# Optimization experiments

Measured on AMD Instinct MI355X. Metric: run time of the kernel, lower is better.

Reference implementation:

```python
import jax, jax.numpy as jnp
import numpy as np

EPS = 1e-5
NEG_SLOPE = 0.01  # F.leaky_relu default


def setup_inputs() -> dict:
    key = jax.random.key(0)
    k1, k2, k3, k4 = jax.random.split(key, 4)
    N, F, H = 8192, 512, 2
    inputs = jax.random.normal(k1, (N, F), dtype=jnp.float32)
    adj = jnp.zeros((N, N), dtype=jnp.float32)  # accepted but unused by the module
    # torch Linear(F, F*H, bias=False): y = x @ W with W of shape [F, F*H]
    W = jax.random.normal(k2, (F, F * H), dtype=jnp.float32) * (1.0 / np.sqrt(F))
    a_w = jax.random.normal(k3, (1,), dtype=jnp.float32)  # Linear(1,1) weight
    a_b = jax.random.normal(k4, (1,), dtype=jnp.float32)  # Linear(1,1) bias
    return {"inputs": inputs, "adj": adj, "W": W, "a_w": a_w, "a_b": a_b}


def reference(inputs, adj, W, a_w, a_b):
    # Wh, Ws = chunk(inputs @ W, 2)
    WhWs = inputs @ W                       # [N, 2F]
    Wh, Ws = jnp.split(WhWs, 2, axis=-1)    # each [N, F]
    # bias = a(ones) = a_w * 1 + a_b  (constant scalar broadcast)
    bias = (a_w + a_b)[0]
    # dense attention: tanh(Wh + Ws + bias) @ Wh^T  -> [N, N]
    scores = jnp.tanh(Wh + Ws + bias) @ Wh.T
    attn = jax.nn.softmax(scores, axis=-1)  # [N, N]
    out = attn @ Wh + inputs                # [N, F] residual
    # training-mode batch norm over node dim, no affine
    mean = jnp.mean(out, axis=0)
    var = jnp.var(out, axis=0)
    out = (out - mean) * jax.lax.rsqrt(var + EPS)
    return jnp.where(out >= 0, out, NEG_SLOPE * out)
```

## Files before the change

kernel.cpp:

```cpp
#include <hip/hip_runtime.h>

using f32x4 = float    __attribute__((ext_vector_type(4)));
using f16x8 = _Float16 __attribute__((ext_vector_type(8)));
using f16x4 = _Float16 __attribute__((ext_vector_type(4)));

__device__ __forceinline__ void gload_lds16(const void* g, void* l) {
    __builtin_amdgcn_global_load_lds(
        (__attribute__((address_space(1))) void*)(void*)g,
        (__attribute__((address_space(3))) void*)l, 16, 0, 0);
}


__global__ __launch_bounds__(256) void k_cvt_x(
    const float* __restrict__ in, _Float16* __restrict__ out) {
    int i = (blockIdx.x * 256 + threadIdx.x) * 8;
    f32x4 a = *(const f32x4*)(in + i);
    f32x4 b = *(const f32x4*)(in + i + 4);
    f16x8 o;
    #pragma unroll
    for (int j = 0; j < 4; ++j) { o[j] = (_Float16)a[j]; o[j + 4] = (_Float16)b[j]; }
    *(f16x8*)(out + i) = o;
}

__global__ __launch_bounds__(256) void k_cvtT(
    const float* __restrict__ in, _Float16* __restrict__ out, int R, int C) {
    __shared__ _Float16 tile[32][33];
    int c0 = blockIdx.x * 32, r0 = blockIdx.y * 32;
    int tx = threadIdx.x & 31, ty = threadIdx.x >> 5;
    #pragma unroll
    for (int i = ty; i < 32; i += 8)
        tile[i][tx] = (_Float16)in[(size_t)(r0 + i) * C + c0 + tx];
    __syncthreads();
    #pragma unroll
    for (int i = ty; i < 32; i += 8)
        out[(size_t)(c0 + i) * R + r0 + tx] = tile[tx][i];
}

__global__ __launch_bounds__(512, 4) void k_gemm1f(
    const _Float16* __restrict__ A, const _Float16* __restrict__ Bt,
    _Float16* __restrict__ Whh, _Float16* __restrict__ T,
    _Float16* __restrict__ WhT,
    const float* __restrict__ aw, const float* __restrict__ ab) {
    __shared__ _Float16 As[128 * 32];
    __shared__ _Float16 B0s[64 * 32];
    __shared__ _Float16 B1s[64 * 32];
    const float bias = aw[0] + ab[0];
    const int row0 = blockIdx.y * 128, col0 = blockIdx.x * 64;
    const int tid = threadIdx.x, w = tid >> 6, lane = tid & 63;
    const int wm = w >> 2, wn = w & 3;
    const int lrow = lane & 15, quad = lane >> 4;
    const int r16 = lane >> 2;
    const int kc = (((lane & 3) - ((lane >> 3) & 3)) & 3) * 8;
    const int sq = ((quad + ((lrow >> 1) & 3)) & 3) * 8;
    f32x4 acc0[4] = {}, acc1[4] = {};
    for (int k0 = 0; k0 < 512; k0 += 32) {
        gload_lds16(A + (size_t)(row0 + w * 16 + r16) * 512 + k0 + kc,
                    As + w * 512);
        if (w < 4)
            gload_lds16(Bt + (size_t)(col0 + w * 16 + r16) * 512 + k0 + kc,
                        B0s + w * 512);
        else
            gload_lds16(Bt + (size_t)(col0 + 512 + (w - 4) * 16 + r16) * 512 + k0 + kc,
                        B1s + (w - 4) * 512);
        __syncthreads();
        f16x8 af[4], b0, b1;
        #pragma unroll
        for (int i = 0; i < 4; ++i)
            af[i] = *(const f16x8*)(As + (wm * 64 + i * 16 + lrow) * 32 + sq);
        b0 = *(const f16x8*)(B0s + (wn * 16 + lrow) * 32 + sq);
        b1 = *(const f16x8*)(B1s + (wn * 16 + lrow) * 32 + sq);
        #pragma unroll
        for (int mi = 0; mi < 4; ++mi) {
            acc0[mi] = __builtin_amdgcn_mfma_f32_16x16x32_f16(af[mi], b0, acc0[mi], 0, 0, 0);
            acc1[mi] = __builtin_amdgcn_mfma_f32_16x16x32_f16(af[mi], b1, acc1[mi], 0, 0, 0);
        }
        __syncthreads();
    }
    const int col = col0 + wn * 16 + lrow;
    #pragma unroll
    for (int mi = 0; mi < 4; ++mi) {
        int rowb = row0 + wm * 64 + mi * 16 + quad * 4;
        f16x4 pw;
        #pragma unroll
        for (int r = 0; r < 4; ++r) {
            float wh = acc0[mi][r];
            float tt = tanhf(wh + acc1[mi][r] + bias);
            Whh[(size_t)(rowb + r) * 512 + col] = (_Float16)wh;
            T[(size_t)(rowb + r) * 512 + col]   = (_Float16)tt;
            pw[r] = (_Float16)wh;
        }
        *(f16x4*)(WhT + (size_t)col * 8192 + rowb) = pw;
    }
}

__global__ __launch_bounds__(512, 4) void k_gemm2(
    const _Float16* __restrict__ A,
    const _Float16* __restrict__ Bt,
    _Float16* __restrict__ Cp) {
    __shared__ _Float16 As[256 * 64];
    __shared__ _Float16 Bs[128 * 64];
    const int row0 = blockIdx.y * 256, col0 = blockIdx.x * 128;
    const int tid = threadIdx.x, w = tid >> 6, lane = tid & 63;
    const int wm = w >> 1, wn = w & 1;
    const int lrow = lane & 15, quad = lane >> 4;
    const int r8 = lane >> 3;
    const int kc8 = (((lane & 7) - r8) & 7) * 8;
    f32x4 acc[4][4] = {};
    for (int k0 = 0; k0 < 512; k0 += 64) {
        #pragma unroll
        for (int i = 0; i < 6; ++i) {
            int c = w + i * 8;
            if (c < 32) {
                gload_lds16(A + (size_t)(row0 + c * 8 + r8) * 512 + k0 + kc8,
                            As + c * 512);
            } else {
                int c2 = c - 32;
                gload_lds16(Bt + (size_t)(col0 + c2 * 8 + r8) * 512 + k0 + kc8,
                            Bs + c2 * 512);
            }
        }
        __syncthreads();
        #pragma unroll
        for (int ks = 0; ks < 2; ++ks) {
            const int sl = ((quad + ks * 4 + lrow) & 7) * 8;
            f16x8 af[4], bf[4];
            #pragma unroll
            for (int i = 0; i < 4; ++i)
                af[i] = *(const f16x8*)(As + (wm * 64 + i * 16 + lrow) * 64 + sl);
            #pragma unroll
            for (int i = 0; i < 4; ++i)
                bf[i] = *(const f16x8*)(Bs + (wn * 64 + i * 16 + lrow) * 64 + sl);
            #pragma unroll
            for (int mi = 0; mi < 4; ++mi)
                #pragma unroll
                for (int ni = 0; ni < 4; ++ni)
                    acc[mi][ni] = __builtin_amdgcn_mfma_f32_16x16x32_f16(
                        af[mi], bf[ni], acc[mi][ni], 0, 0, 0);
        }
        __syncthreads();
    }
    #pragma unroll
    for (int mi = 0; mi < 4; ++mi) {
        #pragma unroll
        for (int ni = 0; ni < 4; ++ni) {
            int col = col0 + wn * 64 + ni * 16 + lrow;
            #pragma unroll
            for (int r = 0; r < 4; ++r) {
                int row = row0 + wm * 64 + mi * 16 + quad * 4 + r;
                Cp[(size_t)row * 8192 + col] = (_Float16)acc[mi][ni][r];
            }
        }
    }
}

__global__ __launch_bounds__(512, 4) void k_gemm3(
    const _Float16* __restrict__ A,
    const _Float16* __restrict__ Bt,
    float* __restrict__ Cp) {
    __shared__ _Float16 As[128 * 64];
    __shared__ _Float16 Bs[256 * 64];
    const int row0 = blockIdx.y * 128, col0 = blockIdx.x * 256;
    const size_t zoff = (size_t)blockIdx.z * 2048;
    Cp += (size_t)blockIdx.z * ((size_t)8192 * 512);
    const int tid = threadIdx.x, w = tid >> 6, lane = tid & 63;
    const int wm = w >> 2, wn = w & 3;
    const int lrow = lane & 15, quad = lane >> 4;
    const int r8 = lane >> 3;
    const int kc8 = (((lane & 7) - r8) & 7) * 8;
    f32x4 acc[4][4] = {};
    for (int k0 = 0; k0 < 2048; k0 += 64) {
        #pragma unroll
        for (int i = 0; i < 6; ++i) {
            int c = w + i * 8;
            if (c < 16) {
                gload_lds16(A + (size_t)(row0 + c * 8 + r8) * 8192 + zoff + k0 + kc8,
                            As + c * 512);
            } else {
                int c2 = c - 16;
                gload_lds16(Bt + (size_t)(col0 + c2 * 8 + r8) * 8192 + zoff + k0 + kc8,
                            Bs + c2 * 512);
            }
        }
        __syncthreads();
        #pragma unroll
        for (int ks = 0; ks < 2; ++ks) {
            const int sl = ((quad + ks * 4 + lrow) & 7) * 8;
            f16x8 af[4], bf[4];
            #pragma unroll
            for (int i = 0; i < 4; ++i)
                af[i] = *(const f16x8*)(As + (wm * 64 + i * 16 + lrow) * 64 + sl);
            #pragma unroll
            for (int i = 0; i < 4; ++i)
                bf[i] = *(const f16x8*)(Bs + (wn * 64 + i * 16 + lrow) * 64 + sl);
            #pragma unroll
            for (int mi = 0; mi < 4; ++mi)
                #pragma unroll
                for (int ni = 0; ni < 4; ++ni)
                    acc[mi][ni] = __builtin_amdgcn_mfma_f32_16x16x32_f16(
                        af[mi], bf[ni], acc[mi][ni], 0, 0, 0);
        }
        __syncthreads();
    }
    #pragma unroll
    for (int mi = 0; mi < 4; ++mi) {
        #pragma unroll
        for (int ni = 0; ni < 4; ++ni) {
            int col = col0 + wn * 64 + ni * 16 + lrow;
            #pragma unroll
            for (int r = 0; r < 4; ++r) {
                int row = row0 + wm * 64 + mi * 16 + quad * 4 + r;
                Cp[(size_t)row * 512 + col] = acc[mi][ni][r];
            }
        }
    }
}

__global__ __launch_bounds__(256) void k_softmax_rows(
    _Float16* __restrict__ S, int N) {
    const int row = blockIdx.x;
    _Float16* prow = S + (size_t)row * N;
    const int t = threadIdx.x;
    float v[32];
    #pragma unroll
    for (int it = 0; it < 4; ++it) {
        f16x8 h = *(const f16x8*)(prow + (it * 256 + t) * 8);
        #pragma unroll
        for (int j = 0; j < 8; ++j) v[it * 8 + j] = (float)h[j];
    }
    float m = v[0];
    #pragma unroll
    for (int j = 1; j < 32; ++j) m = fmaxf(m, v[j]);
    #pragma unroll
    for (int off = 32; off > 0; off >>= 1) m = fmaxf(m, __shfl_xor(m, off));
    __shared__ float red[8];
    const int wid = t >> 6, lane = t & 63;
    if (lane == 0) red[wid] = m;
    __syncthreads();
    m = fmaxf(fmaxf(red[0], red[1]), fmaxf(red[2], red[3]));
    float l = 0.f;
    #pragma unroll
    for (int j = 0; j < 32; ++j) { v[j] = __expf(v[j] - m); l += v[j]; }
    #pragma unroll
    for (int off = 32; off > 0; off >>= 1) l += __shfl_xor(l, off);
    if (lane == 0) red[4 + wid] = l;
    __syncthreads();
    float rl = 1.f / (red[4] + red[5] + red[6] + red[7]);
    #pragma unroll
    for (int it = 0; it < 4; ++it) {
        f16x8 pk;
        #pragma unroll
        for (int j = 0; j < 8; ++j)
            pk[j] = (_Float16)(v[it * 8 + j] * rl);
        *(f16x8*)(prow + (it * 256 + t) * 8) = pk;
    }
}

__global__ __launch_bounds__(256) void k_reduce_stats(
    const float* __restrict__ part, const float* __restrict__ X,
    float* __restrict__ outf, float* __restrict__ cs, float* __restrict__ cq) {
    const int t = threadIdx.x;
    const int r0 = blockIdx.x * 32;
    constexpr size_t PS = (size_t)8192 * 512;
    float s0 = 0, q0 = 0, s1 = 0, q1 = 0;
    for (int r = 0; r < 32; ++r) {
        size_t base = (size_t)(r0 + r) * 512;
        float a = part[base + t] + part[PS + base + t]
                + part[2 * PS + base + t] + part[3 * PS + base + t] + X[base + t];
        float b = part[base + t + 256] + part[PS + base + t + 256]
                + part[2 * PS + base + t + 256] + part[3 * PS + base + t + 256]
                + X[base + t + 256];
        outf[base + t] = a;       outf[base + t + 256] = b;
        s0 += a; q0 += a * a; s1 += b; q1 += b * b;
    }
    atomicAdd(&cs[t], s0);       atomicAdd(&cq[t], q0);
    atomicAdd(&cs[t + 256], s1); atomicAdd(&cq[t + 256], q1);
}

__global__ __launch_bounds__(256) void k_bn_lrelu(
    const float* __restrict__ outf, const float* __restrict__ colsum,
    const float* __restrict__ colsq, float* __restrict__ out) {
    int i = blockIdx.x * 256 + threadIdx.x;
    int c = i & 511;
    constexpr float rN = 1.f / 8192.f;
    float mean = colsum[c] * rN;
    float var  = colsq[c] * rN - mean * mean;
    float y = (outf[i] - mean) * rsqrtf(var + 1e-5f);
    y = (y >= 0.f) ? y : 0.01f * y;
    out[i] = y;
}

extern "C" void kernel_launch(void* const* d_in, const int* in_sizes, int n_in,
                              void* d_out, int out_size, void* d_ws, size_t ws_size,
                              hipStream_t stream) {
    const float* X  = (const float*)d_in[0];
    const float* W  = (const float*)d_in[2];
    const float* aw = (const float*)d_in[3];
    const float* ab = (const float*)d_in[4];
    float* out = (float*)d_out;

    char* ws = (char*)d_ws;
    _Float16* Xh   = (_Float16*)(ws + 0x0);
    _Float16* Wt   = (_Float16*)(ws + 0x800000);
    _Float16* T    = (_Float16*)(ws + 0x900000);
    _Float16* Whh  = (_Float16*)(ws + 0x1100000);
    _Float16* WhT  = (_Float16*)(ws + 0x1900000);
    _Float16* S    = (_Float16*)(ws + 0x2100000);
    float*    outf = (float*)   (ws + 0xA100000);
    float*    part = (float*)   (ws + 0xB100000);
    float*    cs   = (float*)   (ws + 0xF100000);
    float*    cq   = (float*)   (ws + 0xF100800);

    hipMemsetAsync(cs, 0, 4096, stream);
    k_cvt_x<<<dim3((8192 * 512) / 2048), 256, 0, stream>>>(X, Xh);
    k_cvtT<<<dim3(1024 / 32, 512 / 32), 256, 0, stream>>>(W, Wt, 512, 1024);
    k_gemm1f<<<dim3(8, 64), 512, 0, stream>>>(Xh, Wt, Whh, T, WhT, aw, ab);
    k_gemm2<<<dim3(64, 32), 512, 0, stream>>>(T, Whh, S);
    k_softmax_rows<<<dim3(8192), 256, 0, stream>>>(S, 8192);
    k_gemm3<<<dim3(2, 64, 4), 512, 0, stream>>>(S, WhT, part);
    k_reduce_stats<<<dim3(256), 256, 0, stream>>>(part, X, outf, cs, cq);
    k_bn_lrelu<<<dim3((8192 * 512) / 256), 256, 0, stream>>>(outf, cs, cq, out);
}
```

Measured before the change: 511.9 us.

## Fuse softmax into score GEMM epilogue and PV GEMM prologue via partial row stats

Removes the standalone softmax pass over the 8192x8192 half-precision score matrix. The score GEMM now writes per-tile row max and sum-exp partials, a small kernel merges them into per-row max and reciprocal sum, and the PV GEMM applies exp on the fly while staging scores into LDS. The 1/l scaling is deferred to the reduction kernel. This saves a full read and write of the score matrix. In exchange, the PV GEMM loads A through registers instead of async global-to-LDS and recomputes exp, which may slow its main loop. msP/lsP reuse the part buffer region, which is safe because part is written only after those partials are consumed.

```diff
diff --git a/kernel.cpp b/kernel.cpp
--- a/kernel.cpp
+++ b/kernel.cpp
@@ -96,7 +96,8 @@
 __global__ __launch_bounds__(512, 4) void k_gemm2(
     const _Float16* __restrict__ A,
     const _Float16* __restrict__ Bt,
-    _Float16* __restrict__ Cp) {
+    _Float16* __restrict__ Cp,
+    float* __restrict__ msP, float* __restrict__ lsP) {
     __shared__ _Float16 As[256 * 64];
     __shared__ _Float16 Bs[128 * 64];
     const int row0 = blockIdx.y * 256, col0 = blockIdx.x * 128;
@@ -139,23 +140,69 @@
         }
         __syncthreads();
     }
+    const int cb = blockIdx.x * 2 + wn;
     #pragma unroll
     for (int mi = 0; mi < 4; ++mi) {
         #pragma unroll
-        for (int ni = 0; ni < 4; ++ni) {
-            int col = col0 + wn * 64 + ni * 16 + lrow;
-            #pragma unroll
-            for (int r = 0; r < 4; ++r) {
-                int row = row0 + wm * 64 + mi * 16 + quad * 4 + r;
-                Cp[(size_t)row * 8192 + col] = (_Float16)acc[mi][ni][r];
+        for (int r = 0; r < 4; ++r) {
+            const int row = row0 + wm * 64 + mi * 16 + quad * 4 + r;
+            float vq[4]; float sm = -3.0e38f;
+            #pragma unroll
+            for (int ni = 0; ni < 4; ++ni) {
+                _Float16 hv = (_Float16)acc[mi][ni][r];
+                Cp[(size_t)row * 8192 + col0 + wn * 64 + ni * 16 + lrow] = hv;
+                vq[ni] = (float)hv;
+                sm = fmaxf(sm, vq[ni]);
             }
-        }
-    }
+            #pragma unroll
+            for (int off = 1; off < 16; off <<= 1)
+                sm = fmaxf(sm, __shfl_xor(sm, off));
+            float ls = 0.f;
+            #pragma unroll
+            for (int ni = 0; ni < 4; ++ni) ls += __expf(vq[ni] - sm);
+            #pragma unroll
+            for (int off = 1; off < 16; off <<= 1)
+                ls += __shfl_xor(ls, off);
+            if (lrow == 0) {
+                msP[(size_t)cb * 8192 + row] = sm;
+                lsP[(size_t)cb * 8192 + row] = ls;
+            }
+        }
+    }
+}
+
+__global__ __launch_bounds__(64) void k_rowstats(
+    const float* __restrict__ ms, const float* __restrict__ ls,
+    float* __restrict__ mrow, float* __restrict__ rl) {
+    const int row = blockIdx.x * 64 + threadIdx.x;
+    float m[8], l[8];
+    #pragma unroll
+    for (int k = 0; k < 8; ++k) { m[k] = -3.0e38f; l[k] = 0.f; }
+    for (int j = 0; j < 16; ++j) {
+        #pragma unroll
+        for (int k = 0; k < 8; ++k) {
+            const int cb = k * 16 + j;
+            float mb = ms[(size_t)cb * 8192 + row];
+            float lb = ls[(size_t)cb * 8192 + row];
+            float mn = fmaxf(m[k], mb);
+            l[k] = l[k] * __expf(m[k] - mn) + lb * __expf(mb - mn);
+            m[k] = mn;
+        }
+    }
+    float M = m[0];
+    #pragma unroll
+    for (int k = 1; k < 8; ++k) M = fmaxf(M, m[k]);
+    float L = 0.f;
+    #pragma unroll
+    for (int k = 0; k < 8; ++k) L += l[k] * __expf(m[k] - M);
+    mrow[row] = M * 1.44269504f;
+    rl[row]   = 1.f / L;
 }
 
 __global__ __launch_bounds__(512, 4) void k_gemm3(
     const _Float16* __restrict__ A,
     const _Float16* __restrict__ Bt,
+    const float* __restrict__ mrow,
     float* __restrict__ Cp) {
     __shared__ _Float16 As[128 * 64];
     __shared__ _Float16 Bs[256 * 64];
@@ -167,19 +214,27 @@
     const int lrow = lane & 15, quad = lane >> 4;
     const int r8 = lane >> 3;
     const int kc8 = (((lane & 7) - r8) & 7) * 8;
+    const int rowA0 = row0 + w * 8 + r8;
+    const int rowA1 = row0 + (w + 8) * 8 + r8;
+    const float ms0 = mrow[rowA0];
+    const float ms1 = mrow[rowA1];
     f32x4 acc[4][4] = {};
     for (int k0 = 0; k0 < 2048; k0 += 64) {
-        #pragma unroll
-        for (int i = 0; i < 6; ++i) {
-            int c = w + i * 8;
-            if (c < 16) {
-                gload_lds16(A + (size_t)(row0 + c * 8 + r8) * 8192 + zoff + k0 + kc8,
-                            As + c * 512);
-            } else {
-                int c2 = c - 16;
-                gload_lds16(Bt + (size_t)(col0 + c2 * 8 + r8) * 8192 + zoff + k0 + kc8,
-                            Bs + c2 * 512);
-            }
+        f16x8 h0 = *(const f16x8*)(A + (size_t)rowA0 * 8192 + zoff + k0 + kc8);
+        f16x8 h1 = *(const f16x8*)(A + (size_t)rowA1 * 8192 + zoff + k0 + kc8);
+        f16x8 q0, q1;
+        #pragma unroll
+        for (int j = 0; j < 8; ++j) {
+            q0[j] = (_Float16)exp2f(fmaf((float)h0[j], 1.44269504f, -ms0));
+            q1[j] = (_Float16)exp2f(fmaf((float)h1[j], 1.44269504f, -ms1));
+        }
+        *(f16x8*)(As + w * 512 + lane * 8)       = q0;
+        *(f16x8*)(As + (w + 8) * 512 + lane * 8) = q1;
+        #pragma unroll
+        for (int i = 2; i < 6; ++i) {
+            int c2 = w + i * 8 - 16;
+            gload_lds16(Bt + (size_t)(col0 + c2 * 8 + r8) * 8192 + zoff + k0 + kc8,
+                        Bs + c2 * 512);
         }
         __syncthreads();
         #pragma unroll
@@ -215,48 +270,9 @@
     }
 }
 
-__global__ __launch_bounds__(256) void k_softmax_rows(
-    _Float16* __restrict__ S, int N) {
-    const int row = blockIdx.x;
-    _Float16* prow = S + (size_t)row * N;
-    const int t = threadIdx.x;
-    float v[32];
-    #pragma unroll
-    for (int it = 0; it < 4; ++it) {
-        f16x8 h = *(const f16x8*)(prow + (it * 256 + t) * 8);
-        #pragma unroll
-        for (int j = 0; j < 8; ++j) v[it * 8 + j] = (float)h[j];
-    }
-    float m = v[0];
-    #pragma unroll
-    for (int j = 1; j < 32; ++j) m = fmaxf(m, v[j]);
-    #pragma unroll
-    for (int off = 32; off > 0; off >>= 1) m = fmaxf(m, __shfl_xor(m, off));
-    __shared__ float red[8];
-    const int wid = t >> 6, lane = t & 63;
-    if (lane == 0) red[wid] = m;
-    __syncthreads();
-    m = fmaxf(fmaxf(red[0], red[1]), fmaxf(red[2], red[3]));
-    float l = 0.f;
-    #pragma unroll
-    for (int j = 0; j < 32; ++j) { v[j] = __expf(v[j] - m); l += v[j]; }
-    #pragma unroll
-    for (int off = 32; off > 0; off >>= 1) l += __shfl_xor(l, off);
-    if (lane == 0) red[4 + wid] = l;
-    __syncthreads();
-    float rl = 1.f / (red[4] + red[5] + red[6] + red[7]);
-    #pragma unroll
-    for (int it = 0; it < 4; ++it) {
-        f16x8 pk;
-        #pragma unroll
-        for (int j = 0; j < 8; ++j)
-            pk[j] = (_Float16)(v[it * 8 + j] * rl);
-        *(f16x8*)(prow + (it * 256 + t) * 8) = pk;
-    }
-}
-
 __global__ __launch_bounds__(256) void k_reduce_stats(
     const float* __restrict__ part, const float* __restrict__ X,
+    const float* __restrict__ rl,
     float* __restrict__ outf, float* __restrict__ cs, float* __restrict__ cq) {
     const int t = threadIdx.x;
     const int r0 = blockIdx.x * 32;
@@ -264,10 +280,12 @@
     float s0 = 0, q0 = 0, s1 = 0, q1 = 0;
     for (int r = 0; r < 32; ++r) {
         size_t base = (size_t)(r0 + r) * 512;
-        float a = part[base + t] + part[PS + base + t]
-                + part[2 * PS + base + t] + part[3 * PS + base + t] + X[base + t];
-        float b = part[base + t + 256] + part[PS + base + t + 256]
-                + part[2 * PS + base + t + 256] + part[3 * PS + base + t + 256]
+        float rlv = rl[r0 + r];
+        float a = (part[base + t] + part[PS + base + t]
+                + part[2 * PS + base + t] + part[3 * PS + base + t]) * rlv
+                + X[base + t];
+        float b = (part[base + t + 256] + part[PS + base + t + 256]
+                + part[2 * PS + base + t + 256] + part[3 * PS + base + t + 256]) * rlv
                 + X[base + t + 256];
         outf[base + t] = a;       outf[base + t + 256] = b;
         s0 += a; q0 += a * a; s1 += b; q1 += b * b;
@@ -307,16 +325,20 @@
     _Float16* S    = (_Float16*)(ws + 0x2100000);
     float*    outf = (float*)   (ws + 0xA100000);
     float*    part = (float*)   (ws + 0xB100000);
+    float*    msP  = (float*)   (ws + 0xB100000);
+    float*    lsP  = (float*)   (ws + 0xB500000);
     float*    cs   = (float*)   (ws + 0xF100000);
     float*    cq   = (float*)   (ws + 0xF100800);
+    float*    mrow = (float*)   (ws + 0xF101000);
+    float*    rl   = (float*)   (ws + 0xF109000);
 
     hipMemsetAsync(cs, 0, 4096, stream);
     k_cvt_x<<<dim3((8192 * 512) / 2048), 256, 0, stream>>>(X, Xh);
     k_cvtT<<<dim3(1024 / 32, 512 / 32), 256, 0, stream>>>(W, Wt, 512, 1024);
     k_gemm1f<<<dim3(8, 64), 512, 0, stream>>>(Xh, Wt, Whh, T, WhT, aw, ab);
-    k_gemm2<<<dim3(64, 32), 512, 0, stream>>>(T, Whh, S);
-    k_softmax_rows<<<dim3(8192), 256, 0, stream>>>(S, 8192);
-    k_gemm3<<<dim3(2, 64, 4), 512, 0, stream>>>(S, WhT, part);
-    k_reduce_stats<<<dim3(256), 256, 0, stream>>>(part, X, outf, cs, cq);
+    k_gemm2<<<dim3(64, 32), 512, 0, stream>>>(T, Whh, S, msP, lsP);
+    k_rowstats<<<dim3(128), 64, 0, stream>>>(msP, lsP, mrow, rl);
+    k_gemm3<<<dim3(2, 64, 4), 512, 0, stream>>>(S, WhT, mrow, part);
+    k_reduce_stats<<<dim3(256), 256, 0, stream>>>(part, X, rl, outf, cs, cq);
     k_bn_lrelu<<<dim3((8192 * 512) / 256), 256, 0, stream>>>(outf, cs, cq, out);
 }
```

Measured after the change: 535.7 us. 1.05x slower.
